# Optimization experiments

Hardware: AMD Instinct MI355X
Metric: run time of the kernel (lower is better)

## Reference

```python
import jax, jax.numpy as jnp
import numpy as np

B, T, C, H, N = 2, 1024, 2048, 32, 64
KVH = 8                       # GQA kv heads
KV = KVH * N                  # 512
REP = H // KVH                # 4
EPS = 1e-6
LORA = [96, 96, 64, 256, 64]  # xw, xa, xv, xg, xk lora dims


def rmsnorm(x, w, eps=EPS):
    xf = x.astype(jnp.float32)
    var = jnp.mean(xf * xf, axis=-1, keepdims=True)
    return (w * (xf * jax.lax.rsqrt(var + eps))).astype(x.dtype)


def rotate_half(x):
    x1, x2 = jnp.split(x, 2, axis=-1)
    return jnp.concatenate([-x2, x1], axis=-1)


def rwkv7_scan(r, w, k, v, a, b, state0):
    # r,w,k,v,a,b: [B,T,H,N]; state0: [B,H,N,N] (value x key)
    # per step: S = S*exp(w) + (S@a) b^T + v k^T ; o = S @ r
    def step(S, inp):
        r_t, w_t, k_t, v_t, a_t, b_t = inp  # each [B,H,N]
        sa = jnp.einsum('bhvk,bhk->bhv', S, a_t)
        S = (S * jnp.exp(w_t)[:, :, None, :]
             + sa[..., None] * b_t[:, :, None, :]
             + v_t[..., None] * k_t[:, :, None, :])
        o = jnp.einsum('bhvk,bhk->bhv', S, r_t)
        return S, o
    seqs = tuple(jnp.moveaxis(t, 1, 0) for t in (r, w, k, v, a, b))
    S, o = jax.lax.scan(step, state0, seqs)
    return jnp.moveaxis(o, 0, 1), S


def setup_inputs() -> dict:
    key = jax.random.key(0)
    ks = jax.random.split(key, 24)
    g = lambda i, shape, s=0.02: jax.random.normal(ks[i], shape, jnp.float32) * s
    # real rope cache, theta = 1e6, rotary_dim = N
    pos = jnp.arange(T, dtype=jnp.float32)
    inv = 1.0 / (1e6 ** (jnp.arange(0, N, 2, dtype=jnp.float32) / N))
    ang = pos[:, None] * inv[None, :]
    ang = jnp.concatenate([ang, ang], axis=-1)  # [T, N]
    cos = jnp.broadcast_to(jnp.cos(ang)[None], (B, T, N))
    sin = jnp.broadcast_to(jnp.sin(ang)[None], (B, T, N))
    return dict(
        x_in=jax.random.normal(ks[0], (B, T, C), jnp.float32),
        v_first=jax.random.normal(ks[1], (B, T, KVH, N), jnp.float32),
        k_first=jax.random.normal(ks[2], (B, T, KVH, N), jnp.float32),
        state=jnp.zeros((B, H, N, N), jnp.float32),
        calc_cos=cos, calc_sin=sin,
        ln1=jnp.ones((C,), jnp.float32), ln2=jnp.ones((C,), jnp.float32),
        ln_r=jnp.ones((N,), jnp.float32), ln_k=jnp.ones((N,), jnp.float32),
        wavgk1=g(3, (C, sum(LORA))),
        w0=g(4, (H * N,)), w2=g(5, (LORA[0], H * N)),
        a0=g(6, (H * N,)), a2=g(7, (LORA[1], H * N)),
        v0=g(8, (KV,)), v2=g(9, (LORA[2], KV)),
        k0=g(10, (KV,)), k2=g(11, (LORA[4], KV)),
        g2=g(12, (LORA[3], H * N)),
        r_k=g(13, (H, N)),
        RKV_W=g(14, (C, H * N + 2 * KV)),
        O_W=g(15, (H * N, C)),
        R_bias=g(16, (H * N,)), K_bias=g(17, (KV,)), V_bias=g(18, (KV,)),
    )


def _forward(x_in, v_first, k_first, state, calc_cos, calc_sin,
             ln1, ln2, ln_r, ln_k, wavgk1, w0, w2, a0, a2, v0, v2,
             k0, k2, g2, r_k, RKV_W, O_W, R_bias, K_bias, V_bias):
    x = rmsnorm(x_in, ln1)
    xw, xa, xv, xg, xk = jnp.split(x @ wavgk1, np.cumsum(LORA)[:-1].tolist(), axis=-1)
    r, k, v = jnp.split(x @ RKV_W, [H * N, H * N + KV], axis=-1)
    r = (r + R_bias).reshape(B, T, H, N)
    k = (k + K_bias).reshape(B, T, KVH, N)
    v = (v + V_bias).reshape(B, T, KVH, N)
    r = rmsnorm(r, ln_r)
    k = rmsnorm(k, ln_k)
    cos = calc_cos[:, :, None, :]
    sin = calc_sin[:, :, None, :]
    r = r * cos + rotate_half(r) * sin
    k = k * cos + rotate_half(k) * sin
    # layer_id != 0: sigmoid-gated interpolation toward first-layer v/k
    v = v + (v_first - v) * jax.nn.sigmoid(xv @ v2 + v0).reshape(B, T, KVH, N)
    k = k + (k_first - k) * jax.nn.sigmoid(xk @ k2 + k0).reshape(B, T, KVH, N)
    # GQA repeat (contiguous per kv head, as repeat_kv does)
    k = jnp.repeat(k, REP, axis=2).reshape(B, T, H * N)
    v = jnp.repeat(v, REP, axis=2).reshape(B, T, H * N)
    a = jax.nn.sigmoid(xa @ a2 + a0)
    kh = k.reshape(B, T, H, N)
    kk = (kh / (jnp.linalg.norm(kh, axis=-1, keepdims=True) + 1e-12)).reshape(B, T, H * N)
    w = jnp.tanh(xw) @ w2 + w0
    w = -jax.nn.softplus(-w) - 0.5
    k = k * (1.0 - w + a)
    aa = -kk
    bb = kk * a
    wlog = -jnp.exp(w)
    sh = (B, T, H, N)
    o, state = rwkv7_scan(r, wlog.reshape(sh), k.reshape(sh), v.reshape(sh),
                          aa.reshape(sh), bb.reshape(sh), state)
    xx = o.reshape(B, T, H * N) * (float(N) ** -0.5)
    bonus = ((r * k.reshape(sh) * r_k).sum(axis=-1, keepdims=True)
             * v.reshape(sh)).reshape(B, T, H * N)
    xx = xx + bonus
    out = (xx * (jax.nn.sigmoid(xg) @ g2)) @ O_W
    x_res = x_in + out
    output = rmsnorm(x_res, ln2)
    return output, x[:, -1], state, v_first, k_first, x_res


def reference(x_in, v_first, k_first, state, calc_cos, calc_sin,
              ln1, ln2, ln_r, ln_k, wavgk1, w0, w2, a0, a2, v0, v2,
              k0, k2, g2, r_k, RKV_W, O_W, R_bias, K_bias, V_bias):
    return _forward(x_in, v_first, k_first, state, calc_cos, calc_sin,
                    ln1, ln2, ln_r, ln_k, wavgk1, w0, w2, a0, a2, v0, v2,
                    k0, k2, g2, r_k, RKV_W, O_W, R_bias, K_bias, V_bias)
```

## Files before the change

### kernel.cpp

```cpp
#include <hip/hip_runtime.h>
#include <hip/hip_bf16.h>

#define BT 2
#define TT 1024
#define CC 2048
#define HH 32
#define MM (BT*TT)
#define TCH 512
#define NCH (TT/TCH)
#define RECB 896

typedef __attribute__((ext_vector_type(8))) short short8;
typedef __attribute__((ext_vector_type(4))) float floatx4;

static __device__ __forceinline__ float bf2f(__hip_bfloat16 x){ return __bfloat162float(x); }
static __device__ __forceinline__ __hip_bfloat16 f2bf(float x){ return __float2bfloat16(x); }
static __device__ __forceinline__ float sigm(float x){ return 1.0f/(1.0f + expf(-x)); }
static __device__ __forceinline__ float u2f(unsigned short u){
  union { unsigned int i; float f; } x; x.i = ((unsigned int)u) << 16; return x.f;
}
static __device__ __forceinline__ float ulo(unsigned int u){ return __uint_as_float(u << 16); }
static __device__ __forceinline__ float uhi(unsigned int u){ return __uint_as_float(u & 0xffff0000u); }
static __device__ __forceinline__ unsigned short bfbits(float x){
  __hip_bfloat16 h = f2bf(x);
  unsigned short s; __builtin_memcpy(&s, &h, 2); return s;
}
static __device__ __forceinline__ unsigned int pkbf(float lo, float hi){
  return (unsigned int)bfbits(lo) | ((unsigned int)bfbits(hi) << 16);
}

struct u32x3 { unsigned int x, y, z; };

#if defined(__has_builtin)
#if __has_builtin(__builtin_amdgcn_global_load_lds)
#define HAVE_GLL 1
#endif
#endif

#ifdef HAVE_GLL
static __device__ __forceinline__ void gll16(const void* g, void* l){
  __builtin_amdgcn_global_load_lds(
      (__attribute__((address_space(1))) void*)const_cast<void*>(g),
      (__attribute__((address_space(3))) void*)l,
      16, 0, 0);
}
#endif

#define DPP_ADD(x, ctrl) ((x) + __int_as_float(__builtin_amdgcn_update_dpp(0, __float_as_int(x), (ctrl), 0xF, 0xF, true)))

#if defined(__has_builtin)
#if __has_builtin(__builtin_amdgcn_permlane16_swap) && __has_builtin(__builtin_amdgcn_permlane32_swap)
#define HAVE_PLSWAP 1
#endif
#endif

#ifdef HAVE_PLSWAP
typedef unsigned int uint2v __attribute__((ext_vector_type(2)));
static __device__ __forceinline__ float row16_pair_add(float x){
  unsigned int u = __float_as_uint(x);
  uint2v r = __builtin_amdgcn_permlane16_swap(u, u, false, false);
  return __uint_as_float(r[0]) + __uint_as_float(r[1]);
}
static __device__ __forceinline__ float half32_pair_add(float x){
  unsigned int u = __float_as_uint(x);
  uint2v r = __builtin_amdgcn_permlane32_swap(u, u, false, false);
  return __uint_as_float(r[0]) + __uint_as_float(r[1]);
}
#else
static __device__ __forceinline__ float row16_pair_add(float x){ return x + __shfl_xor(x, 16); }
static __device__ __forceinline__ float half32_pair_add(float x){ return x + __shfl_xor(x, 32); }
#endif

static __device__ __forceinline__ float red8(float x){
  x = DPP_ADD(x, 0xB1);
  x = DPP_ADD(x, 0x4E);
  x = DPP_ADD(x, 0x141);
  return x;
}
static __device__ __forceinline__ float red64(float x){
  x = DPP_ADD(x, 0xB1);
  x = DPP_ADD(x, 0x4E);
  x = DPP_ADD(x, 0x124);
  x = DPP_ADD(x, 0x128);
  x = row16_pair_add(x);
  return half32_pair_add(x);
}

__global__ __launch_bounds__(256) void tcvt_kernel(
    const float* __restrict__ W, __hip_bfloat16* __restrict__ Wt,
    int K, int N, int Npad)
{
  __shared__ float tile[32][33];
  const int bn = blockIdx.x*32, bk = blockIdx.y*32;
  const int tx = threadIdx.x & 31, ty0 = threadIdx.x >> 5;
#pragma unroll
  for (int i=0;i<4;++i){
    const int kk = bk + ty0 + i*8;
    float val = 0.f;
    if (kk < K && bn + tx < N) val = W[(size_t)kk*N + bn + tx];
    tile[ty0 + i*8][tx] = val;
  }
  __syncthreads();
#pragma unroll
  for (int i=0;i<4;++i){
    const int nn = bn + ty0 + i*8;
    const int kk = bk + tx;
    if (nn < Npad && kk < K) Wt[(size_t)nn*K + kk] = f2bf(tile[tx][ty0 + i*8]);
  }
}

__global__ __launch_bounds__(256) void rmsnorm1_kernel(
    const float* __restrict__ x_in,
    const float* __restrict__ ln1,
    __hip_bfloat16* __restrict__ x_bf,
    float* __restrict__ x_last)
{
  const int m = blockIdx.x;
  const int tid = threadIdx.x;
  const int c = tid * 8;
  const float* xp = x_in + (size_t)m*CC + c;
  float v[8]; float ss = 0.f;
#pragma unroll
  for (int i=0;i<8;++i){ v[i] = xp[i]; ss += v[i]*v[i]; }
  ss = red64(ss);
  __shared__ float wsum[4];
  if ((tid&63)==0) wsum[tid>>6] = ss;
  __syncthreads();
  ss = wsum[0]+wsum[1]+wsum[2]+wsum[3];
  const float sc = rsqrtf(ss * (1.0f/CC) + 1e-6f);
#pragma unroll
  for (int i=0;i<8;++i) {
    const float y = ln1[c+i] * v[i] * sc;
    x_bf[(size_t)m*CC + c + i] = f2bf(y);
    if ((m % TT) == TT-1) x_last[(size_t)(m/TT)*CC + c + i] = y;
  }
}

template<bool F32OUT, int ACT>
__global__ __launch_bounds__(256) void mgemm(
    const __hip_bfloat16* __restrict__ A, int lda,
    const __hip_bfloat16* __restrict__ Bt,
    void* __restrict__ C, int N, int K)
{
  __shared__ __align__(16) short As[128*32];
  __shared__ __align__(16) short Bs[128*32];
  const int tid = threadIdx.x;
  const int bm = blockIdx.x * 128;
  const int bn = blockIdx.y * 128;
  const int wid = tid >> 6;
  const int lane = tid & 63;
  const int m16 = lane & 15, quad = lane >> 4;
  const int wm = wid & 1, wn = wid >> 1;
  const int lrow = tid >> 2;
  const int lcol = (tid & 3) * 8;

  floatx4 acc[4][4];
#pragma unroll
  for (int i=0;i<4;++i)
#pragma unroll
    for (int j=0;j<4;++j) acc[i][j] = (floatx4){0.f,0.f,0.f,0.f};

  char* asl = (char*)As + tid*16;
  char* bsl = (char*)Bs + tid*16;

  for (int k0 = 0; k0 < K; k0 += 32) {
    __syncthreads();
#ifdef HAVE_GLL
    gll16(A  + (size_t)(bm + lrow)      * lda + k0 + lcol, asl);
    gll16(A  + (size_t)(bm + 64 + lrow) * lda + k0 + lcol, asl + 4096);
    gll16(Bt + (size_t)(bn + lrow)      * K   + k0 + lcol, bsl);
    gll16(Bt + (size_t)(bn + 64 + lrow) * K   + k0 + lcol, bsl + 4096);
#else
    uint4 a0v = *(const uint4*)(const void*)(A  + (size_t)(bm + lrow)      * lda + k0 + lcol);
    uint4 a1v = *(const uint4*)(const void*)(A  + (size_t)(bm + 64 + lrow) * lda + k0 + lcol);
    uint4 b0v = *(const uint4*)(const void*)(Bt + (size_t)(bn + lrow)      * K   + k0 + lcol);
    uint4 b1v = *(const uint4*)(const void*)(Bt + (size_t)(bn + 64 + lrow) * K   + k0 + lcol);
    *(uint4*)(void*)(asl)        = a0v;
    *(uint4*)(void*)(asl + 4096) = a1v;
    *(uint4*)(void*)(bsl)        = b0v;
    *(uint4*)(void*)(bsl + 4096) = b1v;
#endif
    __syncthreads();

    short8 af[4], bfg[4];
#pragma unroll
    for (int mi=0; mi<4; ++mi)
      af[mi] = *(const short8*)(const void*)(As + (wm*64 + mi*16 + m16)*32 + quad*8);
#pragma unroll
    for (int ni=0; ni<4; ++ni)
      bfg[ni] = *(const short8*)(const void*)(Bs + (wn*64 + ni*16 + m16)*32 + quad*8);
#pragma unroll
    for (int mi=0; mi<4; ++mi)
#pragma unroll
      for (int ni=0; ni<4; ++ni)
        acc[mi][ni] = __builtin_amdgcn_mfma_f32_16x16x32_bf16(af[mi], bfg[ni], acc[mi][ni], 0,0,0);
  }

#pragma unroll
  for (int mi=0; mi<4; ++mi) {
    const int row = bm + wm*64 + mi*16 + quad*4;
#pragma unroll
    for (int ni=0; ni<4; ++ni) {
      const int col = bn + wn*64 + ni*16 + m16;
      if (col < N) {
        if (F32OUT) {
          float* cp = (float*)C;
#pragma unroll
          for (int r=0;r<4;++r) cp[(size_t)(row+r)*N + col] = acc[mi][ni][r];
        } else {
          __hip_bfloat16* cp = (__hip_bfloat16*)C;
#pragma unroll
          for (int r=0;r<4;++r) {
            float x = acc[mi][ni][r];
            if (ACT == 1) {
              if (col < 96) x = tanhf(x);
              else if (col >= 256 && col < 512) x = sigm(x);
            }
            cp[(size_t)(row+r)*N + col] = f2bf(x);
          }
        }
      }
    }
  }
}

__global__ __launch_bounds__(256) void prep_kernel(
    const __hip_bfloat16* __restrict__ RKV,
    const __hip_bfloat16* __restrict__ Wpre,
    const __hip_bfloat16* __restrict__ Apre,
    const __hip_bfloat16* __restrict__ Vsig,
    const __hip_bfloat16* __restrict__ Ksig,
    const float* __restrict__ v_first,
    const float* __restrict__ k_first,
    const float* __restrict__ cosp,
    const float* __restrict__ sinp,
    const float* __restrict__ ln_r,
    const float* __restrict__ ln_k,
    const float* __restrict__ r_k,
    const float* __restrict__ w0,
    const float* __restrict__ a0,
    const float* __restrict__ v0,
    const float* __restrict__ k0b,
    const float* __restrict__ R_bias,
    const float* __restrict__ K_bias,
    const float* __restrict__ V_bias,
    char* __restrict__ rec,
    float* __restrict__ bonus,
    int t0)
{
  const int b    = blockIdx.x / TCH;
  const int tloc = blockIdx.x % TCH;
  const int t    = t0 + tloc;
  const int m    = b*TT + t;
  const int tid = threadIdx.x;
  const int h  = tid >> 3;
  const int j  = tid & 7;
  const int hk = h >> 2;
  const int nb = j * 8;
  const int hn = h*64 + nb;
  const int kn = hk*64 + nb;

  const size_t rbase = (size_t)m*3072 + h*64 + nb;
  const size_t kbase = (size_t)m*3072 + 2048 + kn;
  const size_t vbase = kbase + 512;

  float r[8], k[8], v[8];
  float ssr = 0.f, ssk = 0.f;
#pragma unroll
  for (int i=0;i<8;++i) {
    r[i] = bf2f(RKV[rbase+i]) + R_bias[hn+i];
    k[i] = bf2f(RKV[kbase+i]) + K_bias[kn+i];
    v[i] = bf2f(RKV[vbase+i]) + V_bias[kn+i];
    ssr += r[i]*r[i];
    ssk += k[i]*k[i];
  }
  ssr = red8(ssr);
  ssk = red8(ssk);
  const float scr = rsqrtf(ssr*(1.0f/64.0f) + 1e-6f);
  const float sck = rsqrtf(ssk*(1.0f/64.0f) + 1e-6f);
#pragma unroll
  for (int i=0;i<8;++i) {
    r[i] = ln_r[nb+i] * r[i] * scr;
    k[i] = ln_k[nb+i] * k[i] * sck;
  }
  const float sgn = (j < 4) ? -1.0f : 1.0f;
  float rr[8], kr[8];
#pragma unroll
  for (int i=0;i<8;++i) {
    const float cs = cosp[(size_t)m*64 + nb + i];
    const float sn = sinp[(size_t)m*64 + nb + i];
    const float pr = __shfl_xor(r[i], 4);
    const float pk = __shfl_xor(k[i], 4);
    rr[i] = r[i]*cs + sgn*pr*sn;
    kr[i] = k[i]*cs + sgn*pk*sn;
  }
  float av[8], ew[8], wv2[8];
  float ssn = 0.f;
#pragma unroll
  for (int i=0;i<8;++i) {
    const float vs = sigm(bf2f(Vsig[(size_t)m*512 + kn + i]) + v0[kn+i]);
    v[i]  = v[i]  + (v_first[(size_t)m*512 + kn + i] - v[i])  * vs;
    const float ks = sigm(bf2f(Ksig[(size_t)m*512 + kn + i]) + k0b[kn+i]);
    kr[i] = kr[i] + (k_first[(size_t)m*512 + kn + i] - kr[i]) * ks;
    ssn += kr[i]*kr[i];
    av[i] = sigm(bf2f(Apre[(size_t)m*2048 + hn + i]) + a0[hn+i]);
    float wraw = bf2f(Wpre[(size_t)m*2048 + hn + i]) + w0[hn+i];
    const float xs = -wraw;
    const float sp = fmaxf(xs, 0.f) + log1pf(expf(-fabsf(xs)));
    const float wv = -sp - 0.5f;
    wv2[i] = wv;
    ew[i] = expf(-expf(wv));
  }
  ssn = red8(ssn);
  const float inrm = 1.0f / (sqrtf(ssn) + 1e-12f);
  float kf[8], kkv[8];
  float bsum = 0.f;
#pragma unroll
  for (int i=0;i<8;++i) {
    kkv[i] = kr[i] * inrm;
    kf[i]  = kr[i] * (1.0f - wv2[i] + av[i]);
    bsum  += rr[i] * kf[i] * r_k[hn+i];
  }
  bsum = red8(bsum);

  char* base = rec + ((size_t)(b*HH + h)*TCH + tloc)*RECB;
#pragma unroll
  for (int i=0;i<8;++i) {
    u32x3 w;
    w.x = __float_as_uint(ew[i]);
    w.y = pkbf(rr[i], kf[i]);
    w.z = pkbf(kkv[i], -kkv[i]*av[i]);
    *(u32x3*)(void*)(base + (size_t)(nb + i)*12) = w;
  }
  short8 vs8;
#pragma unroll
  for (int i=0;i<8;++i) vs8[i] = (short)bfbits(v[i]);
  *(short8*)(void*)(base + 768 + (size_t)nb*2) = vs8;
#pragma unroll
  for (int i=0;i<8;++i)
    bonus[(size_t)m*2048 + hn + i] = bsum * v[i];
}

__global__ __launch_bounds__(256) void scan_kernel(
    const char* __restrict__ rec,
    float* __restrict__ state,
    float* __restrict__ o_out,
    int t0)
{
  const int blk = blockIdx.x;
  const int bh  = blk & 63;
  const int q   = blk >> 6;
  const int b   = bh >> 5, h = bh & 31;
  const int tid = threadIdx.x;
  const int vl  = q*4 + (tid >> 6);
  const int kl  = tid & 63;

  const char* base = rec + (size_t)bh * TCH * RECB;
  float* sp = state + ((size_t)bh*64 + vl)*64 + kl;
  float S = sp[0];

  const char* pA = base + kl*12;
  const char* pv = base + 768 + vl*2;

  u32x3 Ab[4]; unsigned short vb[4];
#pragma unroll
  for (int s=0;s<4;++s){
    Ab[s] = *(const u32x3*)(const void*)(pA + s*RECB);
    vb[s] = *(const unsigned short*)(const void*)(pv + s*RECB);
  }
  pA += 4*RECB; pv += 4*RECB;

  int oidx = (b*TT + t0)*CC + h*64 + vl - CC;
  float opart = 0.f;

#define SCAN_STEP(jj, PF, ST)                                                  \
  {                                                                            \
    const u32x3 A  = Ab[jj];                                                   \
    const float vf = u2f(vb[jj]);                                              \
    if (PF) {                                                                  \
      Ab[jj] = *(const u32x3*)(const void*)(pA + jj*RECB);                     \
      vb[jj] = *(const unsigned short*)(const void*)(pv + jj*RECB);            \
    }                                                                          \
    float op = red64(opart);                                                   \
    const float kk = ulo(A.z);                                                 \
    float sa = red64(S * kk);                                                  \
    if (ST && kl == 0) o_out[oidx] = op;                                       \
    S = S*__uint_as_float(A.x) + sa*uhi(A.z) + vf*uhi(A.y);                    \
    opart = S * ulo(A.y);                                                      \
    oidx += CC;                                                                \
  }

  SCAN_STEP(0, true, 0)
  SCAN_STEP(1, true, 1)
  SCAN_STEP(2, true, 1)
  SCAN_STEP(3, true, 1)
  pA += 4*RECB; pv += 4*RECB;

  for (int t = 4; t < TCH-4; t += 4) {
    SCAN_STEP(0, true, 1)
    SCAN_STEP(1, true, 1)
    SCAN_STEP(2, true, 1)
    SCAN_STEP(3, true, 1)
    pA += 4*RECB; pv += 4*RECB;
  }
  SCAN_STEP(0, false, 1)
  SCAN_STEP(1, false, 1)
  SCAN_STEP(2, false, 1)
  SCAN_STEP(3, false, 1)
#undef SCAN_STEP

  opart = red64(opart);
  if (kl == 0)
    o_out[oidx] = opart;

  sp[0] = S;
}

__global__ void xxg_kernel(const float* __restrict__ o_in,
                           const float* __restrict__ bonus,
                           const __hip_bfloat16* __restrict__ G,
                           __hip_bfloat16* __restrict__ xxg)
{
  int i = blockIdx.x*256 + threadIdx.x;
  xxg[i] = f2bf((o_in[i]*0.125f + bonus[i]) * bf2f(G[i]));
}

__global__ __launch_bounds__(256) void final_kernel(
    const float* __restrict__ x_in,
    const float* __restrict__ OUTb,
    const float* __restrict__ ln2,
    float* __restrict__ seg0,
    float* __restrict__ seg5)
{
  const int m = blockIdx.x;
  const int tid = threadIdx.x;
  const int c = tid*8;
  const float* xp = x_in + (size_t)m*CC + c;
  const float* op = OUTb + (size_t)m*CC + c;
  float xr[8]; float ss = 0.f;
#pragma unroll
  for (int i=0;i<8;++i){ xr[i] = xp[i] + op[i]; ss += xr[i]*xr[i]; }
#pragma unroll
  for (int i=0;i<8;++i) seg5[(size_t)m*CC + c + i] = xr[i];
  ss = red64(ss);
  __shared__ float wsum[4];
  if ((tid&63)==0) wsum[tid>>6] = ss;
  __syncthreads();
  ss = wsum[0]+wsum[1]+wsum[2]+wsum[3];
  const float sc = rsqrtf(ss*(1.0f/CC) + 1e-6f);
#pragma unroll
  for (int i=0;i<8;++i) seg0[(size_t)m*CC + c + i] = ln2[c+i] * xr[i] * sc;
}

extern "C" void kernel_launch(void* const* d_in, const int* in_sizes, int n_in,
                              void* d_out, int out_size, void* d_ws, size_t ws_size,
                              hipStream_t stream)
{
  (void)in_sizes; (void)n_in; (void)out_size; (void)ws_size;
  const float* x_in   = (const float*)d_in[0];
  const float* v_first= (const float*)d_in[1];
  const float* k_first= (const float*)d_in[2];
  const float* state0 = (const float*)d_in[3];
  const float* cosp   = (const float*)d_in[4];
  const float* sinp   = (const float*)d_in[5];
  const float* ln1    = (const float*)d_in[6];
  const float* ln2    = (const float*)d_in[7];
  const float* ln_r   = (const float*)d_in[8];
  const float* ln_k   = (const float*)d_in[9];
  const float* wavgk1 = (const float*)d_in[10];
  const float* w0     = (const float*)d_in[11];
  const float* w2     = (const float*)d_in[12];
  const float* a0     = (const float*)d_in[13];
  const float* a2     = (const float*)d_in[14];
  const float* v0     = (const float*)d_in[15];
  const float* v2     = (const float*)d_in[16];
  const float* k0b    = (const float*)d_in[17];
  const float* k2     = (const float*)d_in[18];
  const float* g2     = (const float*)d_in[19];
  const float* r_k    = (const float*)d_in[20];
  const float* RKV_W  = (const float*)d_in[21];
  const float* O_W    = (const float*)d_in[22];
  const float* R_bias = (const float*)d_in[23];
  const float* K_bias = (const float*)d_in[24];
  const float* V_bias = (const float*)d_in[25];

  float* out  = (float*)d_out;
  float* seg0 = out;
  float* seg1 = out + 4194304;
  float* seg2 = out + 4198400;
  float* seg3 = out + 4460544;
  float* seg4 = out + 5509120;
  float* seg5 = out + 6557696;

  char* ws = (char*)d_ws;
  const size_t OFF_STF   = 0;
  const size_t OFF_OWT   = 1048576;
  const size_t OFF_G     = 9437184;
  const size_t OFF_VSIG  = 17825792;
  const size_t OFF_KSIG  = 19922944;
  const size_t OFF_WPRE  = 22020096;
  const size_t OFF_APRE  = 30408704;
  const size_t OFF_RKV   = 38797312;
  const size_t OFF_XBF   = 51380224;
  const size_t OFF_Y1    = 59768832;
  const size_t OFF_WT    = 62128128;
  const size_t OFF_WAVT  = OFF_WT;
  const size_t OFF_RKVT  = OFF_WAVT + 2621440;
  const size_t OFF_W2T   = OFF_RKVT + 12582912;
  const size_t OFF_A2T   = OFF_W2T  + 393216;
  const size_t OFF_V2T   = OFF_A2T  + 393216;
  const size_t OFF_K2T   = OFF_V2T  + 65536;
  const size_t OFF_G2T   = OFF_K2T  + 65536;
  const size_t OFF_REC   = OFF_WT;
  const size_t OFF_XXG   = OFF_XBF;
  const size_t OFF_OUT   = OFF_WPRE;

  float*          stf   = (float*)(ws + OFF_STF);
  __hip_bfloat16* owt   = (__hip_bfloat16*)(ws + OFF_OWT);
  __hip_bfloat16* Gbuf  = (__hip_bfloat16*)(ws + OFF_G);
  __hip_bfloat16* Vsig  = (__hip_bfloat16*)(ws + OFF_VSIG);
  __hip_bfloat16* Ksig  = (__hip_bfloat16*)(ws + OFF_KSIG);
  __hip_bfloat16* Wpre  = (__hip_bfloat16*)(ws + OFF_WPRE);
  __hip_bfloat16* Apre  = (__hip_bfloat16*)(ws + OFF_APRE);
  __hip_bfloat16* RKV   = (__hip_bfloat16*)(ws + OFF_RKV);
  __hip_bfloat16* x_bf  = (__hip_bfloat16*)(ws + OFF_XBF);
  __hip_bfloat16* Y1    = (__hip_bfloat16*)(ws + OFF_Y1);
  __hip_bfloat16* wavt  = (__hip_bfloat16*)(ws + OFF_WAVT);
  __hip_bfloat16* rkvt  = (__hip_bfloat16*)(ws + OFF_RKVT);
  __hip_bfloat16* w2t   = (__hip_bfloat16*)(ws + OFF_W2T);
  __hip_bfloat16* a2t   = (__hip_bfloat16*)(ws + OFF_A2T);
  __hip_bfloat16* v2t   = (__hip_bfloat16*)(ws + OFF_V2T);
  __hip_bfloat16* k2t   = (__hip_bfloat16*)(ws + OFF_K2T);
  __hip_bfloat16* g2t   = (__hip_bfloat16*)(ws + OFF_G2T);
  char*           rec   = ws + OFF_REC;
  __hip_bfloat16* xxg   = (__hip_bfloat16*)(ws + OFF_XXG);
  float*          OUTb  = (float*)(ws + OFF_OUT);

  float* o_st = seg0;
  float* b_st = seg5;

  tcvt_kernel<<<dim3(20, 64), 256, 0, stream>>>(wavgk1, wavt, 2048, 576, 640);
  tcvt_kernel<<<dim3(96, 64), 256, 0, stream>>>(RKV_W,  rkvt, 2048, 3072, 3072);
  tcvt_kernel<<<dim3(64, 64), 256, 0, stream>>>(O_W,    owt,  2048, 2048, 2048);
  tcvt_kernel<<<dim3(64,  3), 256, 0, stream>>>(w2,     w2t,    96, 2048, 2048);
  tcvt_kernel<<<dim3(64,  3), 256, 0, stream>>>(a2,     a2t,    96, 2048, 2048);
  tcvt_kernel<<<dim3(16,  2), 256, 0, stream>>>(v2,     v2t,    64,  512,  512);
  tcvt_kernel<<<dim3(16,  2), 256, 0, stream>>>(k2,     k2t,    64,  512,  512);
  tcvt_kernel<<<dim3(64,  8), 256, 0, stream>>>(g2,     g2t,   256, 2048, 2048);

  rmsnorm1_kernel<<<MM, 256, 0, stream>>>(x_in, ln1, x_bf, seg1);
  mgemm<false,1><<<dim3(16,  5), 256, 0, stream>>>(x_bf, CC, wavt, Y1,   576, 2048);
  mgemm<false,0><<<dim3(16, 24), 256, 0, stream>>>(x_bf, CC, rkvt, RKV, 3072, 2048);
  mgemm<false,0><<<dim3(16, 16), 256, 0, stream>>>(Y1+0,   576, w2t, Wpre, 2048, 96);
  mgemm<false,0><<<dim3(16, 16), 256, 0, stream>>>(Y1+96,  576, a2t, Apre, 2048, 96);
  mgemm<false,0><<<dim3(16,  4), 256, 0, stream>>>(Y1+192, 576, v2t, Vsig,  512, 64);
  mgemm<false,0><<<dim3(16,  4), 256, 0, stream>>>(Y1+512, 576, k2t, Ksig,  512, 64);
  mgemm<false,0><<<dim3(16, 16), 256, 0, stream>>>(Y1+256, 576, g2t, Gbuf, 2048, 256);

  hipMemcpyAsync(stf, state0, (size_t)1048576, hipMemcpyDeviceToDevice, stream);
  for (int c = 0; c < NCH; ++c) {
    const int t0 = c*TCH;
    prep_kernel<<<BT*TCH, 256, 0, stream>>>(RKV, Wpre, Apre, Vsig, Ksig, v_first, k_first,
                                            cosp, sinp, ln_r, ln_k, r_k, w0, a0, v0, k0b,
                                            R_bias, K_bias, V_bias, rec, b_st, t0);
    scan_kernel<<<BT*HH*16, 256, 0, stream>>>(rec, stf, o_st, t0);
  }
  hipMemcpyAsync(seg2, stf, (size_t)1048576, hipMemcpyDeviceToDevice, stream);

  xxg_kernel<<<(MM*CC)/256, 256, 0, stream>>>(o_st, b_st, Gbuf, xxg);
  mgemm<true,0><<<dim3(16, 16), 256, 0, stream>>>(xxg, CC, owt, OUTb, 2048, 2048);
  final_kernel<<<MM, 256, 0, stream>>>(x_in, OUTb, ln2, seg0, seg5);

  hipMemcpyAsync(seg3, v_first, (size_t)1048576*4, hipMemcpyDeviceToDevice, stream);
  hipMemcpyAsync(seg4, k_first, (size_t)1048576*4, hipMemcpyDeviceToDevice, stream);
}
```

Baseline: 762.8 us.

## Give each scan thread eight key columns and repack the record layout

Each scan thread now holds eight state elements (one value row, eight key columns) instead of one. The per-step reductions therefore shrink from 64-lane to 8-lane shuffles, and the grid drops to 256 blocks of 128 threads. The prep kernel writes the per-step record as 16-byte and 8-byte packed vectors so the scan can fetch them with wide loads. The catch is far fewer waves to hide the serial dependency chain, plus more registers per thread for double-buffered prefetch.

Measured after the change: 720.3 us. 5.6% less time.

```diff
diff --git a/kernel.cpp b/kernel.cpp
--- a/kernel.cpp
+++ b/kernel.cpp
@@ -28,8 +28,6 @@
 static __device__ __forceinline__ unsigned int pkbf(float lo, float hi){
   return (unsigned int)bfbits(lo) | ((unsigned int)bfbits(hi) << 16);
 }
-
-struct u32x3 { unsigned int x, y, z; };
 
 #if defined(__has_builtin)
 #if __has_builtin(__builtin_amdgcn_global_load_lds)
@@ -324,13 +322,20 @@
   bsum = red8(bsum);
 
   char* base = rec + ((size_t)(b*HH + h)*TCH + tloc)*RECB;
-#pragma unroll
-  for (int i=0;i<8;++i) {
-    u32x3 w;
-    w.x = __float_as_uint(ew[i]);
-    w.y = pkbf(rr[i], kf[i]);
-    w.z = pkbf(kkv[i], -kkv[i]*av[i]);
-    *(u32x3*)(void*)(base + (size_t)(nb + i)*12) = w;
+  const int klb = nb >> 1;
+#pragma unroll
+  for (int p=0;p<4;++p) {
+    const int i0 = 2*p, i1 = i0 + 1;
+    uint4 Aw;
+    Aw.x = __float_as_uint(ew[i0]);
+    Aw.y = __float_as_uint(ew[i1]);
+    Aw.z = pkbf(rr[i0], rr[i1]);
+    Aw.w = pkbf(kf[i0], kf[i1]);
+    *(uint4*)(void*)(base + (size_t)(klb + p)*16) = Aw;
+    uint2 Bw;
+    Bw.x = pkbf(kkv[i0], kkv[i1]);
+    Bw.y = pkbf(-kkv[i0]*av[i0], -kkv[i1]*av[i1]);
+    *(uint2*)(void*)(base + 512 + (size_t)(klb + p)*8) = Bw;
   }
   short8 vs8;
 #pragma unroll
@@ -341,7 +346,7 @@
     bonus[(size_t)m*2048 + hn + i] = bsum * v[i];
 }
 
-__global__ __launch_bounds__(256) void scan_kernel(
+__global__ __launch_bounds__(128) void scan_kernel(
     const char* __restrict__ rec,
     float* __restrict__ state,
     float* __restrict__ o_out,
@@ -352,68 +357,93 @@
   const int q   = blk >> 6;
   const int b   = bh >> 5, h = bh & 31;
   const int tid = threadIdx.x;
-  const int vl  = q*4 + (tid >> 6);
-  const int kl  = tid & 63;
+  const int vl  = q*16 + (tid >> 3);
+  const int g   = tid & 7;
 
   const char* base = rec + (size_t)bh * TCH * RECB;
-  float* sp = state + ((size_t)bh*64 + vl)*64 + kl;
-  float S = sp[0];
-
-  const char* pA = base + kl*12;
+  float* sp = state + ((size_t)bh*64 + vl)*64 + g*8;
+  float S0=sp[0], S1=sp[1], S2=sp[2], S3=sp[3], S4=sp[4], S5=sp[5], S6=sp[6], S7=sp[7];
+
+  const char* pA = base + g*64;
+  const char* pB = base + 512 + g*32;
   const char* pv = base + 768 + vl*2;
 
-  u32x3 Ab[4]; unsigned short vb[4];
-#pragma unroll
-  for (int s=0;s<4;++s){
-    Ab[s] = *(const u32x3*)(const void*)(pA + s*RECB);
-    vb[s] = *(const unsigned short*)(const void*)(pv + s*RECB);
-  }
-  pA += 4*RECB; pv += 4*RECB;
+  uint4 a0x,a1x,a2x,a3x,b0x,b1x, a0y,a1y,a2y,a3y,b0y,b1y;
+  unsigned short vx, vy;
+  a0x = *(const uint4*)(const void*)(pA);
+  a1x = *(const uint4*)(const void*)(pA+16);
+  a2x = *(const uint4*)(const void*)(pA+32);
+  a3x = *(const uint4*)(const void*)(pA+48);
+  b0x = *(const uint4*)(const void*)(pB);
+  b1x = *(const uint4*)(const void*)(pB+16);
+  vx  = *(const unsigned short*)(const void*)(pv);
+  a0y = *(const uint4*)(const void*)(pA+RECB);
+  a1y = *(const uint4*)(const void*)(pA+RECB+16);
+  a2y = *(const uint4*)(const void*)(pA+RECB+32);
+  a3y = *(const uint4*)(const void*)(pA+RECB+48);
+  b0y = *(const uint4*)(const void*)(pB+RECB);
+  b1y = *(const uint4*)(const void*)(pB+RECB+16);
+  vy  = *(const unsigned short*)(const void*)(pv+RECB);
+  pA += 2*RECB; pB += 2*RECB; pv += 2*RECB;
 
   int oidx = (b*TT + t0)*CC + h*64 + vl - CC;
   float opart = 0.f;
 
-#define SCAN_STEP(jj, PF, ST)                                                  \
+#define STEP(A0,A1,A2,A3,B0,B1,VV, PF, PFOFF, ST)                              \
   {                                                                            \
-    const u32x3 A  = Ab[jj];                                                   \
-    const float vf = u2f(vb[jj]);                                              \
+    const float op = red8(opart);                                              \
+                      \
+    float d0 = S0*ulo(B0.x) + S1*uhi(B0.x);                                    \
+    float d1 = S2*ulo(B0.z) + S3*uhi(B0.z);                                    \
+    float d2 = S4*ulo(B1.x) + S5*uhi(B1.x);                                    \
+    float d3 = S6*ulo(B1.z) + S7*uhi(B1.z);                                    \
+    const float sa = red8((d0+d1)+(d2+d3));                                    \
+    if (ST && g == 0) o_out[oidx] = op;                                        \
+    const float vf = u2f(VV);                                                  \
+    S0 = S0*__uint_as_float(A0.x) + sa*ulo(B0.y) + vf*ulo(A0.w);               \
+    S1 = S1*__uint_as_float(A0.y) + sa*uhi(B0.y) + vf*uhi(A0.w);               \
+    S2 = S2*__uint_as_float(A1.x) + sa*ulo(B0.w) + vf*ulo(A1.w);               \
+    S3 = S3*__uint_as_float(A1.y) + sa*uhi(B0.w) + vf*uhi(A1.w);               \
+    S4 = S4*__uint_as_float(A2.x) + sa*ulo(B1.y) + vf*ulo(A2.w);               \
+    S5 = S5*__uint_as_float(A2.y) + sa*uhi(B1.y) + vf*uhi(A2.w);               \
+    S6 = S6*__uint_as_float(A3.x) + sa*ulo(B1.w) + vf*ulo(A3.w);               \
+    S7 = S7*__uint_as_float(A3.y) + sa*uhi(B1.w) + vf*uhi(A3.w);               \
+    float e0 = S0*ulo(A0.z) + S1*uhi(A0.z);                                    \
+    float e1 = S2*ulo(A1.z) + S3*uhi(A1.z);                                    \
+    float e2 = S4*ulo(A2.z) + S5*uhi(A2.z);                                    \
+    float e3 = S6*ulo(A3.z) + S7*uhi(A3.z);                                    \
+    opart = (e0+e1)+(e2+e3);                                                   \
+    oidx += CC;                                                                \
     if (PF) {                                                                  \
-      Ab[jj] = *(const u32x3*)(const void*)(pA + jj*RECB);                     \
-      vb[jj] = *(const unsigned short*)(const void*)(pv + jj*RECB);            \
+      A0 = *(const uint4*)(const void*)(pA + (PFOFF));                         \
+      A1 = *(const uint4*)(const void*)(pA + (PFOFF) + 16);                    \
+      A2 = *(const uint4*)(const void*)(pA + (PFOFF) + 32);                    \
+      A3 = *(const uint4*)(const void*)(pA + (PFOFF) + 48);                    \
+      B0 = *(const uint4*)(const void*)(pB + (PFOFF));                         \
+      B1 = *(const uint4*)(const void*)(pB + (PFOFF) + 16);                    \
+      VV = *(const unsigned short*)(const void*)(pv + (PFOFF));                \
     }                                                                          \
-    float op = red64(opart);                                                   \
-    const float kk = ulo(A.z);                                                 \
-    float sa = red64(S * kk);                                                  \
-    if (ST && kl == 0) o_out[oidx] = op;                                       \
-    S = S*__uint_as_float(A.x) + sa*uhi(A.z) + vf*uhi(A.y);                    \
-    opart = S * ulo(A.y);                                                      \
-    oidx += CC;                                                                \
-  }
-
-  SCAN_STEP(0, true, 0)
-  SCAN_STEP(1, true, 1)
-  SCAN_STEP(2, true, 1)
-  SCAN_STEP(3, true, 1)
-  pA += 4*RECB; pv += 4*RECB;
-
-  for (int t = 4; t < TCH-4; t += 4) {
-    SCAN_STEP(0, true, 1)
-    SCAN_STEP(1, true, 1)
-    SCAN_STEP(2, true, 1)
-    SCAN_STEP(3, true, 1)
-    pA += 4*RECB; pv += 4*RECB;
-  }
-  SCAN_STEP(0, false, 1)
-  SCAN_STEP(1, false, 1)
-  SCAN_STEP(2, false, 1)
-  SCAN_STEP(3, false, 1)
-#undef SCAN_STEP
-
-  opart = red64(opart);
-  if (kl == 0)
-    o_out[oidx] = opart;
-
-  sp[0] = S;
+  }
+
+  STEP(a0x,a1x,a2x,a3x,b0x,b1x,vx, 1, 0,    0)
+  STEP(a0y,a1y,a2y,a3y,b0y,b1y,vy, 1, RECB, 1)
+  pA += 2*RECB; pB += 2*RECB; pv += 2*RECB;
+
+  for (int t = 2; t < TCH-2; t += 2) {
+    STEP(a0x,a1x,a2x,a3x,b0x,b1x,vx, 1, 0,    1)
+    STEP(a0y,a1y,a2y,a3y,b0y,b1y,vy, 1, RECB, 1)
+    pA += 2*RECB; pB += 2*RECB; pv += 2*RECB;
+  }
+  STEP(a0x,a1x,a2x,a3x,b0x,b1x,vx, 0, 0, 1)
+  STEP(a0y,a1y,a2y,a3y,b0y,b1y,vy, 0, 0, 1)
+#undef STEP
+
+  {
+    const float op = red8(opart);
+    if (g == 0) o_out[oidx] = op;
+  }
+
+  sp[0]=S0; sp[1]=S1; sp[2]=S2; sp[3]=S3; sp[4]=S4; sp[5]=S5; sp[6]=S6; sp[7]=S7;
 }
 
 __global__ void xxg_kernel(const float* __restrict__ o_in,
@@ -563,7 +593,7 @@
     prep_kernel<<<BT*TCH, 256, 0, stream>>>(RKV, Wpre, Apre, Vsig, Ksig, v_first, k_first,
                                             cosp, sinp, ln_r, ln_k, r_k, w0, a0, v0, k0b,
                                             R_bias, K_bias, V_bias, rec, b_st, t0);
-    scan_kernel<<<BT*HH*16, 256, 0, stream>>>(rec, stf, o_st, t0);
+    scan_kernel<<<BT*HH*4, 128, 0, stream>>>(rec, stf, o_st, t0);
   }
   hipMemcpyAsync(seg2, stf, (size_t)1048576, hipMemcpyDeviceToDevice, stream);
 
```
